# Kernel optimization log

Measured on AMD Instinct MI355X. Metric: run time of the kernel, lower is better.

The kernel has to match this reference:

```python
import jax, jax.numpy as jnp
import numpy as np

DIM = 256
FOCAL_LEVELS = (3, 5, 7)  # odd kernels so padding=k//2 preserves length
B, L = 8, 16384


def _dwconv(x, k):
    # x: [B, C, L], k: [C, 1, K] depthwise kernel (groups=C)
    pad = k.shape[-1] // 2
    return jax.lax.conv_general_dilated(
        x, k, window_strides=(1,), padding=[(pad, pad)],
        dimension_numbers=('NCH', 'OIH', 'NCH'),
        feature_group_count=x.shape[1])


def setup_inputs() -> dict:
    key = jax.random.key(0)
    ks = jax.random.split(key, 13)
    C = DIM
    G = len(FOCAL_LEVELS) + 1
    s = jnp.float32(0.02)
    inp = {
        'x': jax.random.normal(ks[0], (B, C, L), jnp.float32),
        'q_w': jax.random.normal(ks[1], (C, C), jnp.float32) * s,
        'q_b': jax.random.normal(ks[2], (C,), jnp.float32) * s,
        'v_w': jax.random.normal(ks[3], (C, C), jnp.float32) * s,
        'v_b': jax.random.normal(ks[4], (C,), jnp.float32) * s,
        'g_w': jax.random.normal(ks[5], (G, C), jnp.float32) * s,
        'g_b': jax.random.normal(ks[6], (G,), jnp.float32) * s,
        'f0_w': jax.random.normal(ks[7], (C, 1, FOCAL_LEVELS[0]), jnp.float32) * s,
        'f1_w': jax.random.normal(ks[8], (C, 1, FOCAL_LEVELS[1]), jnp.float32) * s,
        'f2_w': jax.random.normal(ks[9], (C, 1, FOCAL_LEVELS[2]), jnp.float32) * s,
        'mix_w': jax.random.normal(ks[10], (C, C), jnp.float32) * s,
        'mix_b': jax.random.normal(ks[11], (C,), jnp.float32) * s,
    }
    return inp


def reference(x, q_w, q_b, v_w, v_b, g_w, g_b, f0_w, f1_w, f2_w, mix_w, mix_b):
    gelu = lambda t: jax.nn.gelu(t, approximate=False)  # torch GELU default = exact erf
    # Linear weights are [out, in]; contract over channel axis of [B, C, L]
    focus = jnp.einsum('bcl,ec->bel', x, v_w) + v_b[None, :, None]   # [B, C, L]
    gates = jnp.einsum('bcl,gc->bgl', x, g_w) + g_b[None, :, None]   # [B, 4, L]
    query = jnp.einsum('bcl,ec->bel', x, q_w) + q_b[None, :, None]   # [B, C, L]

    kernels = (f0_w, f1_w, f2_w)  # fixed small set: loop over levels is fine
    focus = gelu(_dwconv(focus, kernels[0]))
    acc = focus * gates[:, 0:1, :]
    for i in range(1, len(kernels)):
        focus = gelu(_dwconv(focus, kernels[i]))
        acc = acc + focus * gates[:, i:i + 1, :]

    # global focus: mean over length, GELU, broadcast across length via gate
    global_focus = gelu(jnp.mean(focus, axis=2, keepdims=True))      # [B, C, 1]
    acc = acc + global_focus * gates[:, len(kernels):len(kernels) + 1, :]

    # mix_depth: 1x1 conv == pointwise linear over channels
    acc = jnp.einsum('bcl,oc->bol', acc, mix_w) + mix_b[None, :, None]
    mask = jax.nn.softmax(acc, axis=-1)  # softmax over length
    out = jax.nn.sigmoid(query) * mask
    return (out, mask)
```

## Files before the change

### kernel.cpp

```cpp
#include <hip/hip_runtime.h>

#define LLEN 16384
#define PAD 258

typedef short bf16x8 __attribute__((ext_vector_type(8)));
typedef float f32x4 __attribute__((ext_vector_type(4)));

__device__ __forceinline__ unsigned bfbits(float f) {
  union { float f; unsigned u; } v; v.f = f;
  return (v.u + 0x7FFFu + ((v.u >> 16) & 1u)) >> 16;
}
__device__ __forceinline__ short f2bf(float f) { return (short)bfbits(f); }
__device__ __forceinline__ float bf2f(short s) {
  union { unsigned u; float f; } v;
  v.u = ((unsigned)(unsigned short)s) << 16;
  return v.f;
}
__device__ __forceinline__ float geluf(float x) {
  return 0.5f * x * (1.0f + erff(x * 0.70710678118654752f));
}
__device__ __forceinline__ float gelu_fast(float x) {
  return x / (1.0f + __expf(-1.702f * x));
}
__device__ __forceinline__ float waveRedSum(float v) {
  #pragma unroll
  for (int o = 32; o > 0; o >>= 1) v += __shfl_xor(v, o, 64);
  return v;
}

__global__ __launch_bounds__(256) void k0_convert(
    const float* __restrict__ qw, const float* __restrict__ vw,
    const float* __restrict__ gw, const float* __restrict__ mw,
    short* __restrict__ qwb, short* __restrict__ vwb,
    short* __restrict__ gwb, short* __restrict__ mwb,
    float* __restrict__ rowsum) {
  int idx = blockIdx.x * 256 + threadIdx.x;
  qwb[idx] = f2bf(qw[idx]);
  vwb[idx] = f2bf(vw[idx]);
  mwb[idx] = f2bf(mw[idx]);
  if (idx < 4096) {
    int r = idx >> 8, c = idx & 255;
    gwb[idx] = (r < 4) ? f2bf(gw[r * 256 + c]) : (short)0;
  }
  if (idx < 2048) rowsum[idx] = 0.f;
}

__global__ __launch_bounds__(256) void k0t_transpose(
    const float* __restrict__ x, short* __restrict__ maskS) {
  int tile = blockIdx.x;
  int b = tile >> 8, lt = tile & 255;
  int l0 = lt << 6;
  __shared__ short ts[64][PAD];
  int t = threadIdx.x;
  const float* xb = x + ((size_t)b << 22) + l0;
  int cg = t >> 4;
  int le = (t & 15) * 4;
  #pragma unroll 4
  for (int k = 0; k < 16; ++k) {
    int c = k * 16 + cg;
    float4 v = *(const float4*)&xb[((size_t)c << 14) + le];
    ts[le + 0][c] = f2bf(v.x);
    ts[le + 1][c] = f2bf(v.y);
    ts[le + 2][c] = f2bf(v.z);
    ts[le + 3][c] = f2bf(v.w);
  }
  __syncthreads();
  short* out = maskS + ((size_t)tile << 15) + 16384;
  #pragma unroll
  for (int i = 0; i < 8; ++i) {
    int p = i * 2048 + t * 8;
    *(bf16x8*)&out[p] = *(const bf16x8*)&ts[p >> 8][p & 255];
  }
}

__device__ __forceinline__ void gemm64(const short* __restrict__ wmat,
                                       const short xs[64][PAD], int lane,
                                       f32x4 acc[4][4]) {
  int r = lane & 15, h = lane >> 4;
  #pragma unroll
  for (int k0 = 0; k0 < 256; k0 += 32) {
    bf16x8 xfr[4];
    #pragma unroll
    for (int lf = 0; lf < 4; ++lf)
      xfr[lf] = *(const bf16x8*)&xs[lf * 16 + r][k0 + 8 * h];
    #pragma unroll
    for (int ef = 0; ef < 4; ++ef) {
      bf16x8 wfr = *(const bf16x8*)(wmat + (ef * 16 + r) * 256 + k0 + 8 * h);
      #pragma unroll
      for (int lf = 0; lf < 4; ++lf)
        acc[ef][lf] = __builtin_amdgcn_mfma_f32_16x16x32_bf16(xfr[lf], wfr,
                                                              acc[ef][lf], 0, 0, 0);
    }
  }
}

__device__ __forceinline__ void store_bf4(short* p, f32x4 a, float bias) {
  uint2 pk;
  pk.x = bfbits(a[0] + bias) | (bfbits(a[1] + bias) << 16);
  pk.y = bfbits(a[2] + bias) | (bfbits(a[3] + bias) << 16);
  *(uint2*)p = pk;
}

__global__ __launch_bounds__(256) void k1_qvg(
    const short* __restrict__ xtS, const short* __restrict__ vwb,
    const short* __restrict__ qwb, const short* __restrict__ gwb,
    const float* __restrict__ v_b, const float* __restrict__ q_b,
    const float* __restrict__ g_b, short* __restrict__ focus0,
    short* __restrict__ qzS, float* __restrict__ gates) {
  int b = blockIdx.x >> 8, lt = blockIdx.x & 255;
  int l0 = lt << 6;
  __shared__ short xs[64][PAD];
  int t = threadIdx.x;
  {
    const short* xt = xtS + ((size_t)blockIdx.x << 15) + 16384;
    #pragma unroll
    for (int i = 0; i < 8; ++i) {
      int p = i * 2048 + t * 8;
      *(bf16x8*)&xs[p >> 8][p & 255] = *(const bf16x8*)&xt[p];
    }
  }
  __syncthreads();
  int lane = t & 63, wave = t >> 6;
  int r = lane & 15, h = lane >> 4;
  int e0 = wave << 6;
  f32x4 acc[4][4];

  #pragma unroll
  for (int ef = 0; ef < 4; ++ef)
    #pragma unroll
    for (int lf = 0; lf < 4; ++lf)
      acc[ef][lf] = (f32x4){0.f, 0.f, 0.f, 0.f};
  gemm64(vwb + e0 * 256, xs, lane, acc);
  #pragma unroll
  for (int ef = 0; ef < 4; ++ef) {
    int e = e0 + ef * 16 + r;
    float bias = v_b[e];
    short* rowp = focus0 + ((size_t)((b << 8) | e) << 14) + l0 + 4 * h;
    #pragma unroll
    for (int lf = 0; lf < 4; ++lf)
      store_bf4(rowp + lf * 16, acc[ef][lf], bias);
  }

  #pragma unroll
  for (int ef = 0; ef < 4; ++ef)
    #pragma unroll
    for (int lf = 0; lf < 4; ++lf)
      acc[ef][lf] = (f32x4){0.f, 0.f, 0.f, 0.f};
  gemm64(qwb + e0 * 256, xs, lane, acc);
  #pragma unroll
  for (int ef = 0; ef < 4; ++ef) {
    int e = e0 + ef * 16 + r;
    float bias = q_b[e];
    short* rowp = qzS + (((size_t)((b << 8) | e) << 15) + 16384) + l0 + 4 * h;
    #pragma unroll
    for (int lf = 0; lf < 4; ++lf)
      store_bf4(rowp + lf * 16, acc[ef][lf], bias);
  }

  if (wave == 0) {
    f32x4 gacc[4];
    #pragma unroll
    for (int lf = 0; lf < 4; ++lf) gacc[lf] = (f32x4){0.f, 0.f, 0.f, 0.f};
    #pragma unroll
    for (int k0 = 0; k0 < 256; k0 += 32) {
      bf16x8 wfr = *(const bf16x8*)(gwb + r * 256 + k0 + 8 * h);
      #pragma unroll
      for (int lf = 0; lf < 4; ++lf) {
        bf16x8 xfr = *(const bf16x8*)&xs[lf * 16 + r][k0 + 8 * h];
        gacc[lf] = __builtin_amdgcn_mfma_f32_16x16x32_bf16(xfr, wfr, gacc[lf], 0, 0, 0);
      }
    }
    if (r < 4) {
      float gb = g_b[r];
      float* gp = gates + (((size_t)((b << 2) | r)) << 14) + l0 + 4 * h;
      #pragma unroll
      for (int lf = 0; lf < 4; ++lf) {
        float4 o = {gacc[lf][0] + gb, gacc[lf][1] + gb,
                    gacc[lf][2] + gb, gacc[lf][3] + gb};
        *(float4*)(gp + lf * 16) = o;
      }
    }
  }
}

__global__ __launch_bounds__(256) void k2_conv(
    const short* __restrict__ focus0, const float* __restrict__ gates,
    const float* __restrict__ f0_w, const float* __restrict__ f1_w,
    const float* __restrict__ f2_w, short* __restrict__ acc3S,
    float* __restrict__ rowsum) {
  int bx = blockIdx.x;
  int b = bx >> 12, c = (bx >> 4) & 255, lt = bx & 15;
  int l0 = lt << 10;
  __shared__ float s0[1036], s1[1034], s2[1030];
  __shared__ float rs[4];
  int t = threadIdx.x;
  const short* fp = focus0 + ((size_t)((b << 8) | c) << 14);
  if (lt > 0 && lt < 15) {
    const unsigned* fp2 = (const unsigned*)(fp + l0 - 6);
    for (int i2 = t; i2 < 518; i2 += 256) {
      unsigned u = fp2[i2];
      s0[2 * i2] = bf2f((short)(u & 0xFFFF));
      s0[2 * i2 + 1] = bf2f((short)(u >> 16));
    }
  } else {
    for (int i = t; i < 1036; i += 256) {
      int gl = l0 - 6 + i;
      s0[i] = (gl >= 0 && gl < LLEN) ? bf2f(fp[gl]) : 0.f;
    }
  }
  float w0[3], w1[5], w2[7];
  #pragma unroll
  for (int j = 0; j < 3; ++j) w0[j] = f0_w[c * 3 + j];
  #pragma unroll
  for (int j = 0; j < 5; ++j) w1[j] = f1_w[c * 5 + j];
  #pragma unroll
  for (int j = 0; j < 7; ++j) w2[j] = f2_w[c * 7 + j];
  __syncthreads();
  for (int i = t; i < 1034; i += 256) {
    int gl = l0 - 5 + i;
    float z = w0[0] * s0[i] + w0[1] * s0[i + 1] + w0[2] * s0[i + 2];
    s1[i] = (gl >= 0 && gl < LLEN) ? gelu_fast(z) : 0.f;
  }
  __syncthreads();
  for (int i = t; i < 1030; i += 256) {
    int gl = l0 - 3 + i;
    float z = w1[0] * s1[i] + w1[1] * s1[i + 1] + w1[2] * s1[i + 2] +
              w1[3] * s1[i + 3] + w1[4] * s1[i + 4];
    s2[i] = (gl >= 0 && gl < LLEN) ? gelu_fast(z) : 0.f;
  }
  __syncthreads();
  const float* gp = gates + ((size_t)(b << 2) << 14);
  short* op = acc3S + ((size_t)((b << 8) | c) << 15);
  float lsum = 0.f;
  #pragma unroll
  for (int ii = 0; ii < 2; ++ii) {
    int i = 2 * t + 512 * ii;
    float z0 = w2[0] * s2[i] + w2[1] * s2[i + 1] + w2[2] * s2[i + 2] +
               w2[3] * s2[i + 3] + w2[4] * s2[i + 4] + w2[5] * s2[i + 5] +
               w2[6] * s2[i + 6];
    float z1 = w2[0] * s2[i + 1] + w2[1] * s2[i + 2] + w2[2] * s2[i + 3] +
               w2[3] * s2[i + 4] + w2[4] * s2[i + 5] + w2[5] * s2[i + 6] +
               w2[6] * s2[i + 7];
    float f30 = gelu_fast(z0), f31 = gelu_fast(z1);
    lsum += f30 + f31;
    int l = l0 + i;
    float a0 = s1[i + 5] * gp[l] + s2[i + 3] * gp[LLEN + l] + f30 * gp[2 * LLEN + l];
    float a1 = s1[i + 6] * gp[l + 1] + s2[i + 4] * gp[LLEN + l + 1] +
               f31 * gp[2 * LLEN + l + 1];
    *(unsigned*)&op[l] = bfbits(a0) | (bfbits(a1) << 16);
  }
  float wsv = waveRedSum(lsum);
  if ((t & 63) == 0) rs[t >> 6] = wsv;
  __syncthreads();
  if (t == 0) atomicAdd(&rowsum[(b << 8) | c], rs[0] + rs[1] + rs[2] + rs[3]);
}

__global__ __launch_bounds__(256) void k3b_wgf(
    const float* __restrict__ rowsum, const float* __restrict__ mix_w,
    float* __restrict__ wgf) {
  int b = blockIdx.x;
  int t = threadIdx.x;
  __shared__ float gf_s[256];
  gf_s[t] = geluf(rowsum[(b << 8) | t] * (1.0f / 16384.0f));
  __syncthreads();
  const float* wrow = mix_w + t * 256;
  float s = 0.f;
  #pragma unroll 8
  for (int c = 0; c < 256; ++c) s += wrow[c] * gf_s[c];
  wgf[(b << 8) | t] = s;
}

__global__ __launch_bounds__(256) void k4_mix(
    short* maskS, const float* __restrict__ gates, const float* __restrict__ wgf,
    const short* __restrict__ mwb, const float* __restrict__ mix_b) {
  int b = blockIdx.x >> 8, lt = blockIdx.x & 255;
  int l0 = lt << 6;
  __shared__ short xs[64][PAD];
  int t = threadIdx.x;
  {
    int c = t;
    const unsigned short* arow =
        (const unsigned short*)maskS + (((size_t)((b << 8) | c)) << 15) + l0;
    #pragma unroll
    for (int i = 0; i < 8; ++i) {
      bf16x8 v = *(const bf16x8*)&arow[i * 8];
      #pragma unroll
      for (int j = 0; j < 8; ++j) xs[i * 8 + j][c] = v[j];
    }
  }
  __syncthreads();
  int lane = t & 63, wave = t >> 6;
  int r = lane & 15, h = lane >> 4;
  int e0 = wave << 6;
  f32x4 acc[4][4];
  #pragma unroll
  for (int ef = 0; ef < 4; ++ef)
    #pragma unroll
    for (int lf = 0; lf < 4; ++lf)
      acc[ef][lf] = (f32x4){0.f, 0.f, 0.f, 0.f};
  gemm64(mwb + e0 * 256, xs, lane, acc);
  float4 g3v[4];
  #pragma unroll
  for (int lf = 0; lf < 4; ++lf)
    g3v[lf] = *(const float4*)&gates[(((size_t)((b << 2) | 3)) << 14) + l0 +
                                     lf * 16 + 4 * h];
  #pragma unroll
  for (int ef = 0; ef < 4; ++ef) {
    int o = e0 + ef * 16 + r;
    float base = mix_b[o];
    float wg = wgf[(b << 8) | o];
    short* rowp = maskS + (((size_t)((b << 8) | o) << 15) + 16384) + l0 + 4 * h;
    #pragma unroll
    for (int lf = 0; lf < 4; ++lf) {
      uint2 pk;
      pk.x = bfbits(acc[ef][lf][0] + base + wg * g3v[lf].x) |
             (bfbits(acc[ef][lf][1] + base + wg * g3v[lf].y) << 16);
      pk.y = bfbits(acc[ef][lf][2] + base + wg * g3v[lf].z) |
             (bfbits(acc[ef][lf][3] + base + wg * g3v[lf].w) << 16);
      *(uint2*)(rowp + lf * 16) = pk;
    }
  }
}

__global__ __launch_bounds__(512) void k5_softmax(
    const short* __restrict__ maskS, const short* __restrict__ outS,
    float* __restrict__ maskF, float* __restrict__ outF) {
  int row = blockIdx.x;
  int t = threadIdx.x;
  const short* mrow = maskS + ((size_t)row << 15) + 16384;
  const short* qrow = outS + ((size_t)row << 15) + 16384;
  float* mw = maskF + ((size_t)row << 14);
  float* ow = outF + ((size_t)row << 14);
  int lane = t & 63, wave = t >> 6;
  bf16x8 qv[4];
  float f[32];
  float lm = -3.0e38f;
  #pragma unroll
  for (int i = 0; i < 4; ++i) {
    bf16x8 mv = *(const bf16x8*)&mrow[i * 4096 + t * 8];
    qv[i] = *(const bf16x8*)&qrow[i * 4096 + t * 8];
    #pragma unroll
    for (int j = 0; j < 8; ++j) {
      float vf = bf2f(mv[j]);
      f[i * 8 + j] = vf;
      lm = fmaxf(lm, vf);
    }
  }
  __shared__ float redm[8], reds[8];
  {
    #pragma unroll
    for (int o = 32; o > 0; o >>= 1) lm = fmaxf(lm, __shfl_xor(lm, o, 64));
  }
  if (lane == 0) redm[wave] = lm;
  __syncthreads();
  float M = redm[0];
  #pragma unroll
  for (int w = 1; w < 8; ++w) M = fmaxf(M, redm[w]);
  float ls = 0.f;
  #pragma unroll
  for (int k = 0; k < 32; ++k) {
    f[k] = __expf(f[k] - M);
    ls += f[k];
  }
  float wsum = waveRedSum(ls);
  if (lane == 0) reds[wave] = wsum;
  __syncthreads();
  float S = reds[0];
  #pragma unroll
  for (int w = 1; w < 8; ++w) S += reds[w];
  float inv = 1.0f / S;
  #pragma unroll
  for (int i = 0; i < 4; ++i) {
    float mk[8], oo[8];
    #pragma unroll
    for (int j = 0; j < 8; ++j) {
      mk[j] = f[i * 8 + j] * inv;
      float sig = 1.0f / (1.0f + __expf(-bf2f(qv[i][j])));
      oo[j] = sig * mk[j];
    }
    float* mp = &mw[i * 4096 + t * 8];
    float* op = &ow[i * 4096 + t * 8];
    *(float4*)mp = (float4){mk[0], mk[1], mk[2], mk[3]};
    *(float4*)(mp + 4) = (float4){mk[4], mk[5], mk[6], mk[7]};
    *(float4*)op = (float4){oo[0], oo[1], oo[2], oo[3]};
    *(float4*)(op + 4) = (float4){oo[4], oo[5], oo[6], oo[7]};
  }
}

extern "C" void kernel_launch(void* const* d_in, const int* in_sizes, int n_in,
                              void* d_out, int out_size, void* d_ws, size_t ws_size,
                              hipStream_t stream) {
  const float* x     = (const float*)d_in[0];
  const float* q_w   = (const float*)d_in[1];
  const float* q_b   = (const float*)d_in[2];
  const float* v_w   = (const float*)d_in[3];
  const float* v_b   = (const float*)d_in[4];
  const float* g_w   = (const float*)d_in[5];
  const float* g_b   = (const float*)d_in[6];
  const float* f0_w  = (const float*)d_in[7];
  const float* f1_w  = (const float*)d_in[8];
  const float* f2_w  = (const float*)d_in[9];
  const float* mix_w = (const float*)d_in[10];
  const float* mix_b = (const float*)d_in[11];

  float* outbuf  = (float*)d_out;
  float* maskbuf = outbuf + (size_t)8 * 256 * 16384;
  short* outS  = (short*)outbuf;
  short* maskS = (short*)maskbuf;

  char* ws = (char*)d_ws;
  short* vwb    = (short*)(ws + 0);
  short* qwb    = (short*)(ws + 131072);
  short* mwb    = (short*)(ws + 262144);
  short* gwb    = (short*)(ws + 393216);
  float* rowsum = (float*)(ws + 401408);
  float* wgf    = (float*)(ws + 409600);
  float* gates  = (float*)(ws + 417792);
  short* focus0 = (short*)(ws + 2514944);

  k0_convert<<<dim3(256), dim3(256), 0, stream>>>(q_w, v_w, g_w, mix_w,
                                                  qwb, vwb, gwb, mwb, rowsum);
  k0t_transpose<<<dim3(2048), dim3(256), 0, stream>>>(x, maskS);
  k1_qvg<<<dim3(2048), dim3(256), 0, stream>>>(maskS, vwb, qwb, gwb, v_b, q_b,
                                               g_b, focus0, outS, gates);
  k2_conv<<<dim3(32768), dim3(256), 0, stream>>>(focus0, gates, f0_w, f1_w, f2_w,
                                                 maskS, rowsum);
  k3b_wgf<<<dim3(8), dim3(256), 0, stream>>>(rowsum, mix_w, wgf);
  k4_mix<<<dim3(2048), dim3(256), 0, stream>>>(maskS, gates, wgf, mwb, mix_b);
  k5_softmax<<<dim3(2048), dim3(512), 0, stream>>>(maskS, outS, maskbuf, outbuf);
}
```

Before: 417.4 us.

## Fuse transpose, projections, conv chain and mix GEMM into one kernel

Merges the transpose, q/v/gate projection, three-level depthwise conv chain and the mix GEMM into a single kernel per 64-column tile. Neighbouring tiles' conv halo is recomputed locally: each tile computes v for 76 columns and runs the conv chain from shared memory. The global-focus gate term moves into the softmax kernel, which avoids round trips of focus0, gates and acc3 through global memory. In exchange it does redundant halo GEMM work, uses more shared memory, lowers occupancy and runs a serial per-thread conv loop over 76 positions.

```diff
diff --git a/kernel.cpp b/kernel.cpp
--- a/kernel.cpp
+++ b/kernel.cpp
@@ -21,11 +21,6 @@
 }
 __device__ __forceinline__ float gelu_fast(float x) {
   return x / (1.0f + __expf(-1.702f * x));
-}
-__device__ __forceinline__ float waveRedSum(float v) {
-  #pragma unroll
-  for (int o = 32; o > 0; o >>= 1) v += __shfl_xor(v, o, 64);
-  return v;
 }
 
 __global__ __launch_bounds__(256) void k0_convert(
@@ -45,36 +40,8 @@
   if (idx < 2048) rowsum[idx] = 0.f;
 }
 
-__global__ __launch_bounds__(256) void k0t_transpose(
-    const float* __restrict__ x, short* __restrict__ maskS) {
-  int tile = blockIdx.x;
-  int b = tile >> 8, lt = tile & 255;
-  int l0 = lt << 6;
-  __shared__ short ts[64][PAD];
-  int t = threadIdx.x;
-  const float* xb = x + ((size_t)b << 22) + l0;
-  int cg = t >> 4;
-  int le = (t & 15) * 4;
-  #pragma unroll 4
-  for (int k = 0; k < 16; ++k) {
-    int c = k * 16 + cg;
-    float4 v = *(const float4*)&xb[((size_t)c << 14) + le];
-    ts[le + 0][c] = f2bf(v.x);
-    ts[le + 1][c] = f2bf(v.y);
-    ts[le + 2][c] = f2bf(v.z);
-    ts[le + 3][c] = f2bf(v.w);
-  }
-  __syncthreads();
-  short* out = maskS + ((size_t)tile << 15) + 16384;
-  #pragma unroll
-  for (int i = 0; i < 8; ++i) {
-    int p = i * 2048 + t * 8;
-    *(bf16x8*)&out[p] = *(const bf16x8*)&ts[p >> 8][p & 255];
-  }
-}
-
 __device__ __forceinline__ void gemm64(const short* __restrict__ wmat,
-                                       const short xs[64][PAD], int lane,
+                                       const short (*xs)[PAD], int lane,
                                        f32x4 acc[4][4]) {
   int r = lane & 15, h = lane >> 4;
   #pragma unroll
@@ -101,60 +68,101 @@
   *(uint2*)p = pk;
 }
 
-__global__ __launch_bounds__(256) void k1_qvg(
-    const short* __restrict__ xtS, const short* __restrict__ vwb,
+__global__ __launch_bounds__(256) void kf_fused(
+    const float* __restrict__ x, const short* __restrict__ vwb,
     const short* __restrict__ qwb, const short* __restrict__ gwb,
-    const float* __restrict__ v_b, const float* __restrict__ q_b,
-    const float* __restrict__ g_b, short* __restrict__ focus0,
-    short* __restrict__ qzS, float* __restrict__ gates) {
+    const short* __restrict__ mwb, const float* __restrict__ v_b,
+    const float* __restrict__ q_b, const float* __restrict__ g_b,
+    const float* __restrict__ mix_b, const float* __restrict__ f0_w,
+    const float* __restrict__ f1_w, const float* __restrict__ f2_w,
+    short* __restrict__ qzS, short* __restrict__ mS,
+    float* __restrict__ gates3, float* __restrict__ rowsum) {
   int b = blockIdx.x >> 8, lt = blockIdx.x & 255;
   int l0 = lt << 6;
-  __shared__ short xs[64][PAD];
+  __shared__ short xs[76][PAD];
+  __shared__ short fs[256][82];
   int t = threadIdx.x;
-  {
-    const short* xt = xtS + ((size_t)blockIdx.x << 15) + 16384;
-    #pragma unroll
-    for (int i = 0; i < 8; ++i) {
-      int p = i * 2048 + t * 8;
-      *(bf16x8*)&xs[p >> 8][p & 255] = *(const bf16x8*)&xt[p];
-    }
-  }
-  __syncthreads();
+
+  {
+    int c = t;
+    if (lt != 0 && lt != 255) {
+      const float* xb = x + ((size_t)b << 22) + ((size_t)c << 14) + (l0 - 6);
+      #pragma unroll 4
+      for (int k = 0; k < 38; ++k) {
+        float2 v = *(const float2*)&xb[2 * k];
+        xs[2 * k][c] = f2bf(v.x);
+        xs[2 * k + 1][c] = f2bf(v.y);
+      }
+    } else {
+      const float* xr = x + ((size_t)b << 22) + ((size_t)c << 14);
+      for (int j = 0; j < 76; ++j) {
+        int pos = l0 - 6 + j;
+        xs[j][c] = ((unsigned)pos < (unsigned)LLEN) ? f2bf(xr[pos]) : (short)0;
+      }
+    }
+  }
+  __syncthreads();
+
   int lane = t & 63, wave = t >> 6;
   int r = lane & 15, h = lane >> 4;
   int e0 = wave << 6;
-  f32x4 acc[4][4];
-
-  #pragma unroll
-  for (int ef = 0; ef < 4; ++ef)
-    #pragma unroll
-    for (int lf = 0; lf < 4; ++lf)
-      acc[ef][lf] = (f32x4){0.f, 0.f, 0.f, 0.f};
-  gemm64(vwb + e0 * 256, xs, lane, acc);
-  #pragma unroll
-  for (int ef = 0; ef < 4; ++ef) {
-    int e = e0 + ef * 16 + r;
-    float bias = v_b[e];
-    short* rowp = focus0 + ((size_t)((b << 8) | e) << 14) + l0 + 4 * h;
-    #pragma unroll
-    for (int lf = 0; lf < 4; ++lf)
-      store_bf4(rowp + lf * 16, acc[ef][lf], bias);
-  }
-
-  #pragma unroll
-  for (int ef = 0; ef < 4; ++ef)
-    #pragma unroll
-    for (int lf = 0; lf < 4; ++lf)
-      acc[ef][lf] = (f32x4){0.f, 0.f, 0.f, 0.f};
-  gemm64(qwb + e0 * 256, xs, lane, acc);
-  #pragma unroll
-  for (int ef = 0; ef < 4; ++ef) {
-    int e = e0 + ef * 16 + r;
-    float bias = q_b[e];
-    short* rowp = qzS + (((size_t)((b << 8) | e) << 15) + 16384) + l0 + 4 * h;
-    #pragma unroll
-    for (int lf = 0; lf < 4; ++lf)
-      store_bf4(rowp + lf * 16, acc[ef][lf], bias);
+
+  {
+    f32x4 vacc[4][5];
+    #pragma unroll
+    for (int ef = 0; ef < 4; ++ef)
+      #pragma unroll
+      for (int lf = 0; lf < 5; ++lf)
+        vacc[ef][lf] = (f32x4){0.f, 0.f, 0.f, 0.f};
+    #pragma unroll
+    for (int k0 = 0; k0 < 256; k0 += 32) {
+      bf16x8 xfr[5];
+      #pragma unroll
+      for (int lf = 0; lf < 5; ++lf)
+        xfr[lf] = *(const bf16x8*)&xs[lf * 16 + r][k0 + 8 * h];
+      #pragma unroll
+      for (int ef = 0; ef < 4; ++ef) {
+        bf16x8 wfr = *(const bf16x8*)(vwb + (e0 + ef * 16 + r) * 256 + k0 + 8 * h);
+        #pragma unroll
+        for (int lf = 0; lf < 5; ++lf)
+          vacc[ef][lf] = __builtin_amdgcn_mfma_f32_16x16x32_bf16(xfr[lf], wfr,
+                                                                 vacc[ef][lf], 0, 0, 0);
+      }
+    }
+    #pragma unroll
+    for (int ef = 0; ef < 4; ++ef) {
+      int e = e0 + ef * 16 + r;
+      float bias = v_b[e];
+      #pragma unroll
+      for (int lf = 0; lf < 5; ++lf) {
+        if (lf < 4 || h < 3) {
+          int idx0 = lf * 16 + 4 * h;
+          *(unsigned*)&fs[e][idx0] =
+              bfbits(vacc[ef][lf][0] + bias) | (bfbits(vacc[ef][lf][1] + bias) << 16);
+          *(unsigned*)&fs[e][idx0 + 2] =
+              bfbits(vacc[ef][lf][2] + bias) | (bfbits(vacc[ef][lf][3] + bias) << 16);
+        }
+      }
+    }
+  }
+
+  {
+    f32x4 qacc[4][4];
+    #pragma unroll
+    for (int ef = 0; ef < 4; ++ef)
+      #pragma unroll
+      for (int lf = 0; lf < 4; ++lf)
+        qacc[ef][lf] = (f32x4){0.f, 0.f, 0.f, 0.f};
+    gemm64(qwb + e0 * 256, (const short(*)[PAD])&xs[6], lane, qacc);
+    #pragma unroll
+    for (int ef = 0; ef < 4; ++ef) {
+      int e = e0 + ef * 16 + r;
+      float bias = q_b[e];
+      short* rowp = qzS + (((size_t)((b << 8) | e) << 15) + 16384) + l0 + 4 * h;
+      #pragma unroll
+      for (int lf = 0; lf < 4; ++lf)
+        store_bf4(rowp + lf * 16, qacc[ef][lf], bias);
+    }
   }
 
   if (wave == 0) {
@@ -166,13 +174,22 @@
       bf16x8 wfr = *(const bf16x8*)(gwb + r * 256 + k0 + 8 * h);
       #pragma unroll
       for (int lf = 0; lf < 4; ++lf) {
-        bf16x8 xfr = *(const bf16x8*)&xs[lf * 16 + r][k0 + 8 * h];
+        bf16x8 xfr = *(const bf16x8*)&xs[6 + lf * 16 + r][k0 + 8 * h];
         gacc[lf] = __builtin_amdgcn_mfma_f32_16x16x32_bf16(xfr, wfr, gacc[lf], 0, 0, 0);
       }
     }
-    if (r < 4) {
+    if (r < 3) {
       float gb = g_b[r];
-      float* gp = gates + (((size_t)((b << 2) | r)) << 14) + l0 + 4 * h;
+      #pragma unroll
+      for (int lf = 0; lf < 4; ++lf)
+        #pragma unroll
+        for (int i = 0; i < 4; ++i) {
+          int ci = lf * 16 + 4 * h + i;
+          *(float*)((char*)&fs[ci][0] + 152 + 4 * r) = gacc[lf][i] + gb;
+        }
+    } else if (r == 3) {
+      float gb = g_b[3];
+      float* gp = gates3 + ((size_t)b << 14) + l0 + 4 * h;
       #pragma unroll
       for (int lf = 0; lf < 4; ++lf) {
         float4 o = {gacc[lf][0] + gb, gacc[lf][1] + gb,
@@ -181,78 +198,75 @@
       }
     }
   }
-}
-
-__global__ __launch_bounds__(256) void k2_conv(
-    const short* __restrict__ focus0, const float* __restrict__ gates,
-    const float* __restrict__ f0_w, const float* __restrict__ f1_w,
-    const float* __restrict__ f2_w, short* __restrict__ acc3S,
-    float* __restrict__ rowsum) {
-  int bx = blockIdx.x;
-  int b = bx >> 12, c = (bx >> 4) & 255, lt = bx & 15;
-  int l0 = lt << 10;
-  __shared__ float s0[1036], s1[1034], s2[1030];
-  __shared__ float rs[4];
-  int t = threadIdx.x;
-  const short* fp = focus0 + ((size_t)((b << 8) | c) << 14);
-  if (lt > 0 && lt < 15) {
-    const unsigned* fp2 = (const unsigned*)(fp + l0 - 6);
-    for (int i2 = t; i2 < 518; i2 += 256) {
-      unsigned u = fp2[i2];
-      s0[2 * i2] = bf2f((short)(u & 0xFFFF));
-      s0[2 * i2 + 1] = bf2f((short)(u >> 16));
-    }
-  } else {
-    for (int i = t; i < 1036; i += 256) {
-      int gl = l0 - 6 + i;
-      s0[i] = (gl >= 0 && gl < LLEN) ? bf2f(fp[gl]) : 0.f;
-    }
-  }
-  float w0[3], w1[5], w2[7];
-  #pragma unroll
-  for (int j = 0; j < 3; ++j) w0[j] = f0_w[c * 3 + j];
-  #pragma unroll
-  for (int j = 0; j < 5; ++j) w1[j] = f1_w[c * 5 + j];
-  #pragma unroll
-  for (int j = 0; j < 7; ++j) w2[j] = f2_w[c * 7 + j];
-  __syncthreads();
-  for (int i = t; i < 1034; i += 256) {
-    int gl = l0 - 5 + i;
-    float z = w0[0] * s0[i] + w0[1] * s0[i + 1] + w0[2] * s0[i + 2];
-    s1[i] = (gl >= 0 && gl < LLEN) ? gelu_fast(z) : 0.f;
-  }
-  __syncthreads();
-  for (int i = t; i < 1030; i += 256) {
-    int gl = l0 - 3 + i;
-    float z = w1[0] * s1[i] + w1[1] * s1[i + 1] + w1[2] * s1[i + 2] +
-              w1[3] * s1[i + 3] + w1[4] * s1[i + 4];
-    s2[i] = (gl >= 0 && gl < LLEN) ? gelu_fast(z) : 0.f;
-  }
-  __syncthreads();
-  const float* gp = gates + ((size_t)(b << 2) << 14);
-  short* op = acc3S + ((size_t)((b << 8) | c) << 15);
-  float lsum = 0.f;
-  #pragma unroll
-  for (int ii = 0; ii < 2; ++ii) {
-    int i = 2 * t + 512 * ii;
-    float z0 = w2[0] * s2[i] + w2[1] * s2[i + 1] + w2[2] * s2[i + 2] +
-               w2[3] * s2[i + 3] + w2[4] * s2[i + 4] + w2[5] * s2[i + 5] +
-               w2[6] * s2[i + 6];
-    float z1 = w2[0] * s2[i + 1] + w2[1] * s2[i + 2] + w2[2] * s2[i + 3] +
-               w2[3] * s2[i + 4] + w2[4] * s2[i + 5] + w2[5] * s2[i + 6] +
-               w2[6] * s2[i + 7];
-    float f30 = gelu_fast(z0), f31 = gelu_fast(z1);
-    lsum += f30 + f31;
-    int l = l0 + i;
-    float a0 = s1[i + 5] * gp[l] + s2[i + 3] * gp[LLEN + l] + f30 * gp[2 * LLEN + l];
-    float a1 = s1[i + 6] * gp[l + 1] + s2[i + 4] * gp[LLEN + l + 1] +
-               f31 * gp[2 * LLEN + l + 1];
-    *(unsigned*)&op[l] = bfbits(a0) | (bfbits(a1) << 16);
-  }
-  float wsv = waveRedSum(lsum);
-  if ((t & 63) == 0) rs[t >> 6] = wsv;
-  __syncthreads();
-  if (t == 0) atomicAdd(&rowsum[(b << 8) | c], rs[0] + rs[1] + rs[2] + rs[3]);
+  __syncthreads();
+
+  {
+    int c = t;
+    float w0_[3], w1_[5], w2_[7];
+    #pragma unroll
+    for (int j = 0; j < 3; ++j) w0_[j] = f0_w[c * 3 + j];
+    #pragma unroll
+    for (int j = 0; j < 5; ++j) w1_[j] = f1_w[c * 5 + j];
+    #pragma unroll
+    for (int j = 0; j < 7; ++j) w2_[j] = f2_w[c * 7 + j];
+    float s0a = 0.f, s0b = 0.f, s0c = 0.f;
+    float s1h[6], s2h[7];
+    #pragma unroll
+    for (int j = 0; j < 6; ++j) s1h[j] = 0.f;
+    #pragma unroll
+    for (int j = 0; j < 7; ++j) s2h[j] = 0.f;
+    float lsum = 0.f;
+    #pragma unroll 4
+    for (int idx = 0; idx < 76; ++idx) {
+      int pos = l0 - 6 + idx;
+      float s0v = ((unsigned)pos < (unsigned)LLEN) ? bf2f(fs[c][idx]) : 0.f;
+      s0a = s0b; s0b = s0c; s0c = s0v;
+      float z1 = w0_[0] * s0a + w0_[1] * s0b + w0_[2] * s0c;
+      float s1v = ((unsigned)(pos - 1) < (unsigned)LLEN) ? gelu_fast(z1) : 0.f;
+      s1h[0] = s1h[1]; s1h[1] = s1h[2]; s1h[2] = s1h[3];
+      s1h[3] = s1h[4]; s1h[4] = s1h[5]; s1h[5] = s1v;
+      float z2 = w1_[0] * s1h[1] + w1_[1] * s1h[2] + w1_[2] * s1h[3] +
+                 w1_[3] * s1h[4] + w1_[4] * s1h[5];
+      float s2v = ((unsigned)(pos - 3) < (unsigned)LLEN) ? gelu_fast(z2) : 0.f;
+      s2h[0] = s2h[1]; s2h[1] = s2h[2]; s2h[2] = s2h[3]; s2h[3] = s2h[4];
+      s2h[4] = s2h[5]; s2h[5] = s2h[6]; s2h[6] = s2v;
+      float z3 = w2_[0] * s2h[0] + w2_[1] * s2h[1] + w2_[2] * s2h[2] +
+                 w2_[3] * s2h[3] + w2_[4] * s2h[4] + w2_[5] * s2h[5] +
+                 w2_[6] * s2h[6];
+      float f3v = ((unsigned)(pos - 6) < (unsigned)LLEN) ? gelu_fast(z3) : 0.f;
+      int ci = idx - 12;
+      if ((unsigned)ci < 64u) {
+        lsum += f3v;
+        const char* grow = (const char*)&fs[ci][0];
+        float g0 = *(const float*)(grow + 152);
+        float g1 = *(const float*)(grow + 156);
+        float g2 = *(const float*)(grow + 160);
+        float accv = s1h[0] * g0 + s2h[3] * g1 + f3v * g2;
+        xs[ci][c] = f2bf(accv);
+      }
+    }
+    atomicAdd(&rowsum[(b << 8) | c], lsum);
+  }
+  __syncthreads();
+
+  {
+    f32x4 macc[4][4];
+    #pragma unroll
+    for (int ef = 0; ef < 4; ++ef)
+      #pragma unroll
+      for (int lf = 0; lf < 4; ++lf)
+        macc[ef][lf] = (f32x4){0.f, 0.f, 0.f, 0.f};
+    gemm64(mwb + e0 * 256, (const short(*)[PAD])&xs[0], lane, macc);
+    #pragma unroll
+    for (int ef = 0; ef < 4; ++ef) {
+      int o = e0 + ef * 16 + r;
+      float base = mix_b[o];
+      short* rowp = mS + (((size_t)((b << 8) | o) << 15) + 16384) + l0 + 4 * h;
+      #pragma unroll
+      for (int lf = 0; lf < 4; ++lf)
+        store_bf4(rowp + lf * 16, macc[ef][lf], base);
+    }
+  }
 }
 
 __global__ __launch_bounds__(256) void k3b_wgf(
@@ -270,65 +284,17 @@
   wgf[(b << 8) | t] = s;
 }
 
-__global__ __launch_bounds__(256) void k4_mix(
-    short* maskS, const float* __restrict__ gates, const float* __restrict__ wgf,
-    const short* __restrict__ mwb, const float* __restrict__ mix_b) {
-  int b = blockIdx.x >> 8, lt = blockIdx.x & 255;
-  int l0 = lt << 6;
-  __shared__ short xs[64][PAD];
-  int t = threadIdx.x;
-  {
-    int c = t;
-    const unsigned short* arow =
-        (const unsigned short*)maskS + (((size_t)((b << 8) | c)) << 15) + l0;
-    #pragma unroll
-    for (int i = 0; i < 8; ++i) {
-      bf16x8 v = *(const bf16x8*)&arow[i * 8];
-      #pragma unroll
-      for (int j = 0; j < 8; ++j) xs[i * 8 + j][c] = v[j];
-    }
-  }
-  __syncthreads();
-  int lane = t & 63, wave = t >> 6;
-  int r = lane & 15, h = lane >> 4;
-  int e0 = wave << 6;
-  f32x4 acc[4][4];
-  #pragma unroll
-  for (int ef = 0; ef < 4; ++ef)
-    #pragma unroll
-    for (int lf = 0; lf < 4; ++lf)
-      acc[ef][lf] = (f32x4){0.f, 0.f, 0.f, 0.f};
-  gemm64(mwb + e0 * 256, xs, lane, acc);
-  float4 g3v[4];
-  #pragma unroll
-  for (int lf = 0; lf < 4; ++lf)
-    g3v[lf] = *(const float4*)&gates[(((size_t)((b << 2) | 3)) << 14) + l0 +
-                                     lf * 16 + 4 * h];
-  #pragma unroll
-  for (int ef = 0; ef < 4; ++ef) {
-    int o = e0 + ef * 16 + r;
-    float base = mix_b[o];
-    float wg = wgf[(b << 8) | o];
-    short* rowp = maskS + (((size_t)((b << 8) | o) << 15) + 16384) + l0 + 4 * h;
-    #pragma unroll
-    for (int lf = 0; lf < 4; ++lf) {
-      uint2 pk;
-      pk.x = bfbits(acc[ef][lf][0] + base + wg * g3v[lf].x) |
-             (bfbits(acc[ef][lf][1] + base + wg * g3v[lf].y) << 16);
-      pk.y = bfbits(acc[ef][lf][2] + base + wg * g3v[lf].z) |
-             (bfbits(acc[ef][lf][3] + base + wg * g3v[lf].w) << 16);
-      *(uint2*)(rowp + lf * 16) = pk;
-    }
-  }
-}
-
 __global__ __launch_bounds__(512) void k5_softmax(
     const short* __restrict__ maskS, const short* __restrict__ outS,
+    const float* __restrict__ gates3, const float* __restrict__ wgf,
     float* __restrict__ maskF, float* __restrict__ outF) {
   int row = blockIdx.x;
+  int b = row >> 8;
   int t = threadIdx.x;
   const short* mrow = maskS + ((size_t)row << 15) + 16384;
   const short* qrow = outS + ((size_t)row << 15) + 16384;
+  const float* g3r = gates3 + ((size_t)b << 14);
+  float wg = wgf[row];
   float* mw = maskF + ((size_t)row << 14);
   float* ow = outF + ((size_t)row << 14);
   int lane = t & 63, wave = t >> 6;
@@ -339,9 +305,12 @@
   for (int i = 0; i < 4; ++i) {
     bf16x8 mv = *(const bf16x8*)&mrow[i * 4096 + t * 8];
     qv[i] = *(const bf16x8*)&qrow[i * 4096 + t * 8];
+    float4 ga = *(const float4*)&g3r[i * 4096 + t * 8];
+    float4 gb = *(const float4*)&g3r[i * 4096 + t * 8 + 4];
+    float gj[8] = {ga.x, ga.y, ga.z, ga.w, gb.x, gb.y, gb.z, gb.w};
     #pragma unroll
     for (int j = 0; j < 8; ++j) {
-      float vf = bf2f(mv[j]);
+      float vf = bf2f(mv[j]) + wg * gj[j];
       f[i * 8 + j] = vf;
       lm = fmaxf(lm, vf);
     }
@@ -362,8 +331,11 @@
     f[k] = __expf(f[k] - M);
     ls += f[k];
   }
-  float wsum = waveRedSum(ls);
-  if (lane == 0) reds[wave] = wsum;
+  {
+    #pragma unroll
+    for (int o = 32; o > 0; o >>= 1) ls += __shfl_xor(ls, o, 64);
+  }
+  if (lane == 0) reds[wave] = ls;
   __syncthreads();
   float S = reds[0];
   #pragma unroll
@@ -415,17 +387,15 @@
   short* gwb    = (short*)(ws + 393216);
   float* rowsum = (float*)(ws + 401408);
   float* wgf    = (float*)(ws + 409600);
-  float* gates  = (float*)(ws + 417792);
-  short* focus0 = (short*)(ws + 2514944);
+  float* gates3 = (float*)(ws + 417792);
 
   k0_convert<<<dim3(256), dim3(256), 0, stream>>>(q_w, v_w, g_w, mix_w,
                                                   qwb, vwb, gwb, mwb, rowsum);
-  k0t_transpose<<<dim3(2048), dim3(256), 0, stream>>>(x, maskS);
-  k1_qvg<<<dim3(2048), dim3(256), 0, stream>>>(maskS, vwb, qwb, gwb, v_b, q_b,
-                                               g_b, focus0, outS, gates);
-  k2_conv<<<dim3(32768), dim3(256), 0, stream>>>(focus0, gates, f0_w, f1_w, f2_w,
-                                                 maskS, rowsum);
+  kf_fused<<<dim3(2048), dim3(256), 0, stream>>>(x, vwb, qwb, gwb, mwb,
+                                                 v_b, q_b, g_b, mix_b,
+                                                 f0_w, f1_w, f2_w,
+                                                 outS, maskS, gates3, rowsum);
   k3b_wgf<<<dim3(8), dim3(256), 0, stream>>>(rowsum, mix_w, wgf);
-  k4_mix<<<dim3(2048), dim3(256), 0, stream>>>(maskS, gates, wgf, mwb, mix_b);
-  k5_softmax<<<dim3(2048), dim3(512), 0, stream>>>(maskS, outS, maskbuf, outbuf);
-}
+  k5_softmax<<<dim3(2048), dim3(512), 0, stream>>>(maskS, outS, gates3, wgf,
+                                                   maskbuf, outbuf);
+}
```

After: 388.9 us. 6.8% less time.

## Fuse input transpose into QVG GEMM, enlarge mix tiles, use fast reciprocals

Applied to the files above, without the earlier changes.

Removes the separate transpose kernel. k1 now reads fp32 x directly, converts it to bf16 and transposes it into LDS, which saves one global write and read of the transposed activations. k1 and k4 go to 512-thread blocks covering 128 positions each, and the k4 load packs channel pairs into 32-bit LDS stores instead of scalar 16-bit scatters. Divisions in gelu_fast, the sigmoid and the softmax normalisation are replaced with v_rcp_f32 (plus a Newton step for the sum), at a small cost in accuracy. The larger blocks use about 66KB of LDS each, which may reduce occupancy.

```diff
diff --git a/kernel.cpp b/kernel.cpp
--- a/kernel.cpp
+++ b/kernel.cpp
@@ -16,11 +16,16 @@
   v.u = ((unsigned)(unsigned short)s) << 16;
   return v.f;
 }
+__device__ __forceinline__ float fastrcp(float x) {
+  float r;
+  asm("v_rcp_f32 %0, %1" : "=v"(r) : "v"(x));
+  return r;
+}
 __device__ __forceinline__ float geluf(float x) {
   return 0.5f * x * (1.0f + erff(x * 0.70710678118654752f));
 }
 __device__ __forceinline__ float gelu_fast(float x) {
-  return x / (1.0f + __expf(-1.702f * x));
+  return x * fastrcp(1.0f + __expf(-1.702f * x));
 }
 __device__ __forceinline__ float waveRedSum(float v) {
   #pragma unroll
@@ -45,36 +50,8 @@
   if (idx < 2048) rowsum[idx] = 0.f;
 }
 
-__global__ __launch_bounds__(256) void k0t_transpose(
-    const float* __restrict__ x, short* __restrict__ maskS) {
-  int tile = blockIdx.x;
-  int b = tile >> 8, lt = tile & 255;
-  int l0 = lt << 6;
-  __shared__ short ts[64][PAD];
-  int t = threadIdx.x;
-  const float* xb = x + ((size_t)b << 22) + l0;
-  int cg = t >> 4;
-  int le = (t & 15) * 4;
-  #pragma unroll 4
-  for (int k = 0; k < 16; ++k) {
-    int c = k * 16 + cg;
-    float4 v = *(const float4*)&xb[((size_t)c << 14) + le];
-    ts[le + 0][c] = f2bf(v.x);
-    ts[le + 1][c] = f2bf(v.y);
-    ts[le + 2][c] = f2bf(v.z);
-    ts[le + 3][c] = f2bf(v.w);
-  }
-  __syncthreads();
-  short* out = maskS + ((size_t)tile << 15) + 16384;
-  #pragma unroll
-  for (int i = 0; i < 8; ++i) {
-    int p = i * 2048 + t * 8;
-    *(bf16x8*)&out[p] = *(const bf16x8*)&ts[p >> 8][p & 255];
-  }
-}
-
 __device__ __forceinline__ void gemm64(const short* __restrict__ wmat,
-                                       const short xs[64][PAD], int lane,
+                                       const short (*xs)[PAD], int lane,
                                        f32x4 acc[4][4]) {
   int r = lane & 15, h = lane >> 4;
   #pragma unroll
@@ -101,28 +78,37 @@
   *(uint2*)p = pk;
 }
 
-__global__ __launch_bounds__(256) void k1_qvg(
-    const short* __restrict__ xtS, const short* __restrict__ vwb,
+__global__ __launch_bounds__(512) void k1_qvg(
+    const float* __restrict__ x, const short* __restrict__ vwb,
     const short* __restrict__ qwb, const short* __restrict__ gwb,
     const float* __restrict__ v_b, const float* __restrict__ q_b,
     const float* __restrict__ g_b, short* __restrict__ focus0,
     short* __restrict__ qzS, float* __restrict__ gates) {
-  int b = blockIdx.x >> 8, lt = blockIdx.x & 255;
-  int l0 = lt << 6;
-  __shared__ short xs[64][PAD];
+  int b = blockIdx.x >> 7, lt = blockIdx.x & 127;
+  int l0 = lt << 7;
+  __shared__ short xs[128][PAD];
   int t = threadIdx.x;
   {
-    const short* xt = xtS + ((size_t)blockIdx.x << 15) + 16384;
-    #pragma unroll
-    for (int i = 0; i < 8; ++i) {
-      int p = i * 2048 + t * 8;
-      *(bf16x8*)&xs[p >> 8][p & 255] = *(const bf16x8*)&xt[p];
+    int lq = (t & 31) * 4, cg = t >> 5;
+    const float* xb = x + ((size_t)b << 22) + l0 + lq;
+    #pragma unroll
+    for (int rep = 0; rep < 8; ++rep) {
+      int c = rep * 32 + cg * 2;
+      float4 va = *(const float4*)&xb[(size_t)c << 14];
+      float4 vb = *(const float4*)&xb[((size_t)c + 1) << 14];
+      *(unsigned*)&xs[lq + 0][c] = bfbits(va.x) | (bfbits(vb.x) << 16);
+      *(unsigned*)&xs[lq + 1][c] = bfbits(va.y) | (bfbits(vb.y) << 16);
+      *(unsigned*)&xs[lq + 2][c] = bfbits(va.z) | (bfbits(vb.z) << 16);
+      *(unsigned*)&xs[lq + 3][c] = bfbits(va.w) | (bfbits(vb.w) << 16);
     }
   }
   __syncthreads();
   int lane = t & 63, wave = t >> 6;
+  int we = wave & 3, wl = wave >> 2;
   int r = lane & 15, h = lane >> 4;
-  int e0 = wave << 6;
+  int e0 = we << 6;
+  const short (*xsl)[PAD] = (const short (*)[PAD])&xs[wl << 6];
+  int lbase = l0 + (wl << 6) + 4 * h;
   f32x4 acc[4][4];
 
   #pragma unroll
@@ -130,12 +116,12 @@
     #pragma unroll
     for (int lf = 0; lf < 4; ++lf)
       acc[ef][lf] = (f32x4){0.f, 0.f, 0.f, 0.f};
-  gemm64(vwb + e0 * 256, xs, lane, acc);
+  gemm64(vwb + e0 * 256, xsl, lane, acc);
   #pragma unroll
   for (int ef = 0; ef < 4; ++ef) {
     int e = e0 + ef * 16 + r;
     float bias = v_b[e];
-    short* rowp = focus0 + ((size_t)((b << 8) | e) << 14) + l0 + 4 * h;
+    short* rowp = focus0 + ((size_t)((b << 8) | e) << 14) + lbase;
     #pragma unroll
     for (int lf = 0; lf < 4; ++lf)
       store_bf4(rowp + lf * 16, acc[ef][lf], bias);
@@ -146,18 +132,18 @@
     #pragma unroll
     for (int lf = 0; lf < 4; ++lf)
       acc[ef][lf] = (f32x4){0.f, 0.f, 0.f, 0.f};
-  gemm64(qwb + e0 * 256, xs, lane, acc);
+  gemm64(qwb + e0 * 256, xsl, lane, acc);
   #pragma unroll
   for (int ef = 0; ef < 4; ++ef) {
     int e = e0 + ef * 16 + r;
     float bias = q_b[e];
-    short* rowp = qzS + (((size_t)((b << 8) | e) << 15) + 16384) + l0 + 4 * h;
+    short* rowp = qzS + (((size_t)((b << 8) | e) << 15) + 16384) + lbase;
     #pragma unroll
     for (int lf = 0; lf < 4; ++lf)
       store_bf4(rowp + lf * 16, acc[ef][lf], bias);
   }
 
-  if (wave == 0) {
+  if (we == 0) {
     f32x4 gacc[4];
     #pragma unroll
     for (int lf = 0; lf < 4; ++lf) gacc[lf] = (f32x4){0.f, 0.f, 0.f, 0.f};
@@ -166,13 +152,13 @@
       bf16x8 wfr = *(const bf16x8*)(gwb + r * 256 + k0 + 8 * h);
       #pragma unroll
       for (int lf = 0; lf < 4; ++lf) {
-        bf16x8 xfr = *(const bf16x8*)&xs[lf * 16 + r][k0 + 8 * h];
+        bf16x8 xfr = *(const bf16x8*)&xsl[lf * 16 + r][k0 + 8 * h];
         gacc[lf] = __builtin_amdgcn_mfma_f32_16x16x32_bf16(xfr, wfr, gacc[lf], 0, 0, 0);
       }
     }
     if (r < 4) {
       float gb = g_b[r];
-      float* gp = gates + (((size_t)((b << 2) | r)) << 14) + l0 + 4 * h;
+      float* gp = gates + (((size_t)((b << 2) | r)) << 14) + lbase;
       #pragma unroll
       for (int lf = 0; lf < 4; ++lf) {
         float4 o = {gacc[lf][0] + gb, gacc[lf][1] + gb,
@@ -270,46 +256,53 @@
   wgf[(b << 8) | t] = s;
 }
 
-__global__ __launch_bounds__(256) void k4_mix(
+__global__ __launch_bounds__(512) void k4_mix(
     short* maskS, const float* __restrict__ gates, const float* __restrict__ wgf,
     const short* __restrict__ mwb, const float* __restrict__ mix_b) {
-  int b = blockIdx.x >> 8, lt = blockIdx.x & 255;
-  int l0 = lt << 6;
-  __shared__ short xs[64][PAD];
+  int b = blockIdx.x >> 7, lt = blockIdx.x & 127;
+  int l0 = lt << 7;
+  __shared__ short xs[128][PAD];
   int t = threadIdx.x;
   {
-    int c = t;
-    const unsigned short* arow =
-        (const unsigned short*)maskS + (((size_t)((b << 8) | c)) << 15) + l0;
-    #pragma unroll
-    for (int i = 0; i < 8; ++i) {
-      bf16x8 v = *(const bf16x8*)&arow[i * 8];
-      #pragma unroll
-      for (int j = 0; j < 8; ++j) xs[i * 8 + j][c] = v[j];
+    int lq = (t & 31) * 4, cg = t >> 5;
+    const unsigned short* base =
+        (const unsigned short*)maskS + (((size_t)(b << 8)) << 15) + l0 + lq;
+    #pragma unroll
+    for (int rep = 0; rep < 8; ++rep) {
+      int c = rep * 32 + cg * 2;
+      uint2 av = *(const uint2*)&base[(size_t)c << 15];
+      uint2 bv = *(const uint2*)&base[((size_t)c + 1) << 15];
+      *(unsigned*)&xs[lq + 0][c] = (av.x & 0xFFFF) | (bv.x << 16);
+      *(unsigned*)&xs[lq + 1][c] = (av.x >> 16) | (bv.x & 0xFFFF0000u);
+      *(unsigned*)&xs[lq + 2][c] = (av.y & 0xFFFF) | (bv.y << 16);
+      *(unsigned*)&xs[lq + 3][c] = (av.y >> 16) | (bv.y & 0xFFFF0000u);
     }
   }
   __syncthreads();
   int lane = t & 63, wave = t >> 6;
+  int we = wave & 3, wl = wave >> 2;
   int r = lane & 15, h = lane >> 4;
-  int e0 = wave << 6;
+  int e0 = we << 6;
+  const short (*xsl)[PAD] = (const short (*)[PAD])&xs[wl << 6];
+  int lbase = l0 + (wl << 6) + 4 * h;
   f32x4 acc[4][4];
   #pragma unroll
   for (int ef = 0; ef < 4; ++ef)
     #pragma unroll
     for (int lf = 0; lf < 4; ++lf)
       acc[ef][lf] = (f32x4){0.f, 0.f, 0.f, 0.f};
-  gemm64(mwb + e0 * 256, xs, lane, acc);
+  gemm64(mwb + e0 * 256, xsl, lane, acc);
   float4 g3v[4];
   #pragma unroll
   for (int lf = 0; lf < 4; ++lf)
-    g3v[lf] = *(const float4*)&gates[(((size_t)((b << 2) | 3)) << 14) + l0 +
-                                     lf * 16 + 4 * h];
+    g3v[lf] = *(const float4*)&gates[(((size_t)((b << 2) | 3)) << 14) + lbase +
+                                     lf * 16];
   #pragma unroll
   for (int ef = 0; ef < 4; ++ef) {
     int o = e0 + ef * 16 + r;
     float base = mix_b[o];
     float wg = wgf[(b << 8) | o];
-    short* rowp = maskS + (((size_t)((b << 8) | o) << 15) + 16384) + l0 + 4 * h;
+    short* rowp = maskS + (((size_t)((b << 8) | o) << 15) + 16384) + lbase;
     #pragma unroll
     for (int lf = 0; lf < 4; ++lf) {
       uint2 pk;
@@ -368,14 +361,14 @@
   float S = reds[0];
   #pragma unroll
   for (int w = 1; w < 8; ++w) S += reds[w];
-  float inv = 1.0f / S;
+  float inv = fastrcp(S) * (2.0f - S * fastrcp(S));
   #pragma unroll
   for (int i = 0; i < 4; ++i) {
     float mk[8], oo[8];
     #pragma unroll
     for (int j = 0; j < 8; ++j) {
       mk[j] = f[i * 8 + j] * inv;
-      float sig = 1.0f / (1.0f + __expf(-bf2f(qv[i][j])));
+      float sig = fastrcp(1.0f + __expf(-bf2f(qv[i][j])));
       oo[j] = sig * mk[j];
     }
     float* mp = &mw[i * 4096 + t * 8];
@@ -420,12 +413,11 @@
 
   k0_convert<<<dim3(256), dim3(256), 0, stream>>>(q_w, v_w, g_w, mix_w,
                                                   qwb, vwb, gwb, mwb, rowsum);
-  k0t_transpose<<<dim3(2048), dim3(256), 0, stream>>>(x, maskS);
-  k1_qvg<<<dim3(2048), dim3(256), 0, stream>>>(maskS, vwb, qwb, gwb, v_b, q_b,
-                                               g_b, focus0, outS, gates);
+  k1_qvg<<<dim3(1024), dim3(512), 0, stream>>>(x, vwb, qwb, gwb, v_b, q_b, g_b,
+                                               focus0, outS, gates);
   k2_conv<<<dim3(32768), dim3(256), 0, stream>>>(focus0, gates, f0_w, f1_w, f2_w,
                                                  maskS, rowsum);
   k3b_wgf<<<dim3(8), dim3(256), 0, stream>>>(rowsum, mix_w, wgf);
-  k4_mix<<<dim3(2048), dim3(256), 0, stream>>>(maskS, gates, wgf, mwb, mix_b);
+  k4_mix<<<dim3(1024), dim3(512), 0, stream>>>(maskS, gates, wgf, mwb, mix_b);
   k5_softmax<<<dim3(2048), dim3(512), 0, stream>>>(maskS, outS, maskbuf, outbuf);
 }
```

Measured after the change: 377.9 us. 9.5% less time.
